# Optimization experiments

Hardware: AMD Instinct MI355X
Metric: run time of the kernel (lower is better)

The kernel has to match this reference:

```python
import jax, jax.numpy as jnp
import numpy as np

SCALE = 32.0 / 16.0  # alpha / r

def setup_inputs() -> dict:
    key = jax.random.key(0)
    k1, k2, k3, k4, k5 = jax.random.split(key, 5)
    B, S, D_in, D_out, R = 4, 4096, 4096, 4096, 16
    x = jax.random.normal(k1, (B, S, D_in), dtype=jnp.float32)
    W = jax.random.normal(k2, (D_out, D_in), dtype=jnp.float32) * 0.02
    b = jax.random.normal(k3, (D_out,), dtype=jnp.float32) * 0.02
    lora_A = jax.random.normal(k4, (D_in, R), dtype=jnp.float32) * 0.01
    lora_B = jax.random.normal(k5, (R, D_out), dtype=jnp.float32) * 0.01
    return {"x": x, "W": W, "b": b, "lora_A": lora_A, "lora_B": lora_B}

def reference(x, W, b, lora_A, lora_B):
    # base: x @ W.T + b  (nn.Linear semantics: weight is [out_f, in_f])
    out = jnp.einsum("bsd,od->bso", x, W) + b
    # LoRA path: (x @ A) @ B, scaled residual add
    lora = jnp.einsum("bsr,ro->bso", jnp.einsum("bsd,dr->bsr", x, lora_A), lora_B)
    return out + SCALE * lora
```

## Files before the change

kernel.cpp:

```cpp
#include <hip/hip_runtime.h>
#include <hip/hip_bf16.h>

typedef __bf16 bf16_t;
typedef __bf16 bf16x8 __attribute__((ext_vector_type(8)));
typedef __bf16 bf16x4 __attribute__((ext_vector_type(4)));
typedef float floatx4 __attribute__((ext_vector_type(4)));

#define M_DIM 16384
#define N_DIM 4096
#define K_DIM 4096
#define R_DIM 16
#define LORA_SCALE 2.0f

__device__ __forceinline__ void async_copy16(void* lds, const void* gptr) {
  __builtin_amdgcn_global_load_lds(
      (__attribute__((address_space(1))) void*)(gptr),
      (__attribute__((address_space(3))) void*)(lds),
      16, 0, 0);
}

__device__ __forceinline__ void block_barrier() {
  asm volatile("" ::: "memory");
  __builtin_amdgcn_s_barrier();
  asm volatile("" ::: "memory");
}

__global__ void cvt_kernel(const float* __restrict__ src,
                           bf16_t* __restrict__ dst, int n8) {
  const int idx = blockIdx.x * blockDim.x + threadIdx.x;
  if (idx >= n8) return;
  const float4 a = ((const float4*)src)[idx * 2 + 0];
  const float4 b = ((const float4*)src)[idx * 2 + 1];
  bf16x8 v;
  v[0] = (bf16_t)a.x; v[1] = (bf16_t)a.y; v[2] = (bf16_t)a.z; v[3] = (bf16_t)a.w;
  v[4] = (bf16_t)b.x; v[5] = (bf16_t)b.y; v[6] = (bf16_t)b.z; v[7] = (bf16_t)b.w;
  ((bf16x8*)dst)[idx] = v;
}

__launch_bounds__(256, 2)
__global__ void lora_xa_bf16(const bf16_t* __restrict__ X,
                             const float* __restrict__ A,
                             bf16_t* __restrict__ T) {
  __shared__ bf16_t Xs[64 * 64];
  __shared__ bf16_t At[16 * 64];
  const int tid  = threadIdx.x;
  const int wave = tid >> 6;
  const int lane = tid & 63;
  const int quad = lane >> 4;
  const int l15  = lane & 15;
  const int gm0  = blockIdx.x * 64;

  floatx4 acc = {0.f, 0.f, 0.f, 0.f};
  for (int k0 = 0; k0 < K_DIM; k0 += 64) {
#pragma unroll
    for (int j = 0; j < 2; ++j) {
      const int i   = wave * 2 + j;
      const int row = i * 8 + (lane >> 3);
      const int col = (lane & 7) * 8;
      async_copy16(&Xs[i * 512], X + (size_t)(gm0 + row) * K_DIM + k0 + col);
    }
    {
      const int c  = tid >> 4;
      const int k4 = (tid & 15) * 4;
#pragma unroll
      for (int j = 0; j < 4; ++j)
        At[c * 64 + k4 + j] = (bf16_t)A[(size_t)(k0 + k4 + j) * R_DIM + c];
    }
    __syncthreads();
#pragma unroll
    for (int h = 0; h < 2; ++h) {
      const int kk = h * 32;
      const bf16x8 a = *(const bf16x8*)&Xs[(wave * 16 + l15) * 64 + kk + quad * 8];
      const bf16x8 b = *(const bf16x8*)&At[l15 * 64 + kk + quad * 8];
      acc = __builtin_amdgcn_mfma_f32_16x16x32_bf16(a, b, acc, 0, 0, 0);
    }
    __syncthreads();
  }
#pragma unroll
  for (int r = 0; r < 4; ++r) {
    const int row = gm0 + wave * 16 + quad * 4 + r;
    T[(size_t)row * R_DIM + l15] = (bf16_t)(LORA_SCALE * acc[r]);
  }
}

__launch_bounds__(256, 2)
__global__ void lora_xa_f32(const float* __restrict__ X,
                            const float* __restrict__ A,
                            bf16_t* __restrict__ T) {
  __shared__ bf16_t Xs[64 * 64];
  __shared__ bf16_t At[16 * 64];
  const int tid  = threadIdx.x;
  const int wave = tid >> 6;
  const int lane = tid & 63;
  const int quad = lane >> 4;
  const int l15  = lane & 15;
  const int gm0  = blockIdx.x * 64;

  floatx4 acc = {0.f, 0.f, 0.f, 0.f};
  for (int k0 = 0; k0 < K_DIM; k0 += 64) {
#pragma unroll
    for (int i = 0; i < 4; ++i) {
      const int idx  = tid + i * 256;
      const int row  = idx >> 4;
      const int colf = idx & 15;
      const float4 v = *(const float4*)&X[(size_t)(gm0 + row) * K_DIM + k0 + colf * 4];
      bf16x4 w;
      w[0] = (bf16_t)v.x; w[1] = (bf16_t)v.y; w[2] = (bf16_t)v.z; w[3] = (bf16_t)v.w;
      *(bf16x4*)&Xs[row * 64 + colf * 4] = w;
    }
    {
      const int c  = tid >> 4;
      const int k4 = (tid & 15) * 4;
#pragma unroll
      for (int j = 0; j < 4; ++j)
        At[c * 64 + k4 + j] = (bf16_t)A[(size_t)(k0 + k4 + j) * R_DIM + c];
    }
    __syncthreads();
#pragma unroll
    for (int h = 0; h < 2; ++h) {
      const int kk = h * 32;
      const bf16x8 a = *(const bf16x8*)&Xs[(wave * 16 + l15) * 64 + kk + quad * 8];
      const bf16x8 b = *(const bf16x8*)&At[l15 * 64 + kk + quad * 8];
      acc = __builtin_amdgcn_mfma_f32_16x16x32_bf16(a, b, acc, 0, 0, 0);
    }
    __syncthreads();
  }
#pragma unroll
  for (int r = 0; r < 4; ++r) {
    const int row = gm0 + wave * 16 + quad * 4 + r;
    T[(size_t)row * R_DIM + l15] = (bf16_t)(LORA_SCALE * acc[r]);
  }
}

#define LD_A(AQ)                                                               \
  _Pragma("unroll") for (int i_ = 0; i_ < 4; ++i_) {                           \
    const int r_ = (rowA + ((AQ) * 4 + i_) * 16) * 64;                         \
    af[i_][0] = *(const bf16x8*)&Ab[r_ + ((quad    ) ^ swz) * 8];              \
    af[i_][1] = *(const bf16x8*)&Ab[r_ + ((quad + 4) ^ swz) * 8];              \
  }

#define LD_B(BQ)                                                               \
  _Pragma("unroll") for (int j_ = 0; j_ < 2; ++j_) {                           \
    const int r_ = (rowB + ((BQ) * 2 + j_) * 16) * 64;                         \
    bfr[j_][0] = *(const bf16x8*)&Bb[r_ + ((quad    ) ^ swz) * 8];             \
    bfr[j_][1] = *(const bf16x8*)&Bb[r_ + ((quad + 4) ^ swz) * 8];             \
  }

#define MFMA16(AQ, BQ)                                                         \
  __builtin_amdgcn_s_setprio(1);                                               \
  _Pragma("unroll") for (int i_ = 0; i_ < 4; ++i_)                             \
  _Pragma("unroll") for (int j_ = 0; j_ < 2; ++j_) {                           \
    acc[(AQ) * 4 + i_][(BQ) * 2 + j_] =                                        \
        __builtin_amdgcn_mfma_f32_16x16x32_bf16(                               \
            af[i_][0], bfr[j_][0], acc[(AQ) * 4 + i_][(BQ) * 2 + j_], 0, 0, 0);\
    acc[(AQ) * 4 + i_][(BQ) * 2 + j_] =                                        \
        __builtin_amdgcn_mfma_f32_16x16x32_bf16(                               \
            af[i_][1], bfr[j_][1], acc[(AQ) * 4 + i_][(BQ) * 2 + j_], 0, 0, 0);\
  }                                                                            \
  __builtin_amdgcn_s_setprio(0);

__launch_bounds__(512, 2)
__global__ void main8_bf16(const bf16_t* __restrict__ X,
                           const bf16_t* __restrict__ W,
                           const float* __restrict__ bias,
                           const float* __restrict__ loraB,
                           const bf16_t* __restrict__ T,
                           float* __restrict__ out) {
  extern __shared__ bf16_t lds[];
  bf16_t* As = lds;
  bf16_t* Bs = lds + 32768;

  const int tid  = threadIdx.x;
  const int wave = tid >> 6;
  const int lane = tid & 63;
  const int quad = lane >> 4;
  const int l15  = lane & 15;
  const int swz  = l15 & 7;
  const int wr   = wave >> 2;
  const int wc   = wave & 3;

  const int b   = blockIdx.x;
  const int swb = (b & 7) * 128 + (b >> 3);
  const int gm  = (swb >> 4) * 256;
  const int gn  = (swb & 15) * 256;

  const int rowA = wr * 128 + l15;
  const int rowB = wc * 64 + l15;

  const int srow  = wave * 8 + (lane >> 3);
  const int sslot = (lane & 7) ^ ((lane >> 3) & 7);
  const bf16_t* gA = X + (size_t)(gm + srow) * K_DIM + sslot * 8;
  const bf16_t* gB = W + (size_t)(gn + srow) * K_DIM + sslot * 8;

  auto stageA = [&](int bsel, int u, int t) {
    async_copy16(As + bsel * 16384 + u * 4096 + wave * 512,
                 gA + (size_t)u * 64 * K_DIM + t * 64);
  };
  auto stageB = [&](int bsel, int u, int t) {
    async_copy16(Bs + bsel * 16384 + u * 4096 + wave * 512,
                 gB + (size_t)u * 64 * K_DIM + t * 64);
  };

  floatx4 acc[8][4];
#pragma unroll
  for (int i = 0; i < 8; ++i)
#pragma unroll
    for (int j = 0; j < 4; ++j) acc[i][j] = (floatx4){0.f, 0.f, 0.f, 0.f};

#pragma unroll
  for (int u = 0; u < 4; ++u) stageA(0, u, 0);
#pragma unroll
  for (int u = 0; u < 4; ++u) stageB(0, u, 0);
  stageA(1, 0, 1); stageA(1, 2, 1);
  asm volatile("s_waitcnt vmcnt(2)" ::: "memory");
  block_barrier();

  const int NITER = K_DIM / 128;
  for (int i = 0; i < NITER; ++i) {
    const int t1 = 2 * i + 1, t2 = 2 * i + 2, t3 = 2 * i + 3;
    const bool last = (i == NITER - 1);
    bf16x8 af[4][2];
    bf16x8 bfr[2][2];

    {
      const bf16_t* Ab = As;
      const bf16_t* Bb = Bs;
      LD_A(0); LD_B(0);
      stageA(1, 1, t1); stageA(1, 3, t1);
      stageB(1, 0, t1); stageB(1, 1, t1); stageB(1, 2, t1); stageB(1, 3, t1);
      block_barrier(); MFMA16(0, 0); block_barrier();
      LD_B(1);
      block_barrier(); MFMA16(0, 1); block_barrier();
      LD_A(1);
      if (!last) { stageA(0, 0, t2); stageA(0, 2, t2); }
      block_barrier(); MFMA16(1, 1); block_barrier();
      LD_B(0);
      block_barrier(); MFMA16(1, 0);
      if (last) asm volatile("s_waitcnt vmcnt(0)" ::: "memory");
      else      asm volatile("s_waitcnt vmcnt(2)" ::: "memory");
      block_barrier();
    }
    {
      const bf16_t* Ab = As + 16384;
      const bf16_t* Bb = Bs + 16384;
      LD_A(0); LD_B(0);
      if (!last) {
        stageA(0, 1, t2); stageA(0, 3, t2);
        stageB(0, 0, t2); stageB(0, 1, t2); stageB(0, 2, t2); stageB(0, 3, t2);
      }
      block_barrier(); MFMA16(0, 0); block_barrier();
      LD_B(1);
      block_barrier(); MFMA16(0, 1); block_barrier();
      LD_A(1);
      if (!last) { stageA(1, 0, t3); stageA(1, 2, t3); }
      block_barrier(); MFMA16(1, 1); block_barrier();
      LD_B(0);
      block_barrier(); MFMA16(1, 0);
      if (last) asm volatile("s_waitcnt vmcnt(0)" ::: "memory");
      else      asm volatile("s_waitcnt vmcnt(2)" ::: "memory");
      block_barrier();
    }
  }

  if (tid < 256) {
    const int row = tid;
    const bf16_t* tp = T + (size_t)(gm + row) * R_DIM;
    *(uint4*)&As[row * 32]      = *(const uint4*)tp;
    *(uint4*)&As[row * 32 + 8]  = *(const uint4*)(tp + 8);
    *(uint4*)&As[row * 32 + 16] = make_uint4(0, 0, 0, 0);
    *(uint4*)&As[row * 32 + 24] = make_uint4(0, 0, 0, 0);
  } else {
    const int n = tid - 256;
#pragma unroll
    for (int r = 0; r < R_DIM; ++r)
      Bs[n * 32 + r] = (bf16_t)loraB[(size_t)r * N_DIM + gn + n];
    *(uint4*)&Bs[n * 32 + 16] = make_uint4(0, 0, 0, 0);
    *(uint4*)&Bs[n * 32 + 24] = make_uint4(0, 0, 0, 0);
  }
  __syncthreads();
  {
    bf16x8 afr[8]; bf16x8 bft[4];
#pragma unroll
    for (int im = 0; im < 8; ++im)
      afr[im] = *(const bf16x8*)&As[(wr * 128 + im * 16 + l15) * 32 + quad * 8];
#pragma unroll
    for (int in = 0; in < 4; ++in)
      bft[in] = *(const bf16x8*)&Bs[(wc * 64 + in * 16 + l15) * 32 + quad * 8];
#pragma unroll
    for (int im = 0; im < 8; ++im)
#pragma unroll
      for (int in = 0; in < 4; ++in)
        acc[im][in] = __builtin_amdgcn_mfma_f32_16x16x32_bf16(
            afr[im], bft[in], acc[im][in], 0, 0, 0);
  }

#pragma unroll
  for (int in = 0; in < 4; ++in) {
    const int col = gn + wc * 64 + in * 16 + l15;
    const float bv = bias[col];
#pragma unroll
    for (int im = 0; im < 8; ++im) {
      const int row0 = gm + wr * 128 + im * 16 + quad * 4;
#pragma unroll
      for (int r = 0; r < 4; ++r)
        out[(size_t)(row0 + r) * N_DIM + col] = acc[im][in][r] + bv;
    }
  }
}

__launch_bounds__(256, 2)
__global__ void main_f32(const float* __restrict__ X,
                         const float* __restrict__ W,
                         const float* __restrict__ bias,
                         const float* __restrict__ loraB,
                         const bf16_t* __restrict__ T,
                         float* __restrict__ out) {
  __shared__ bf16_t As[128 * 32];
  __shared__ bf16_t Bs[128 * 32];
  const int tid  = threadIdx.x;
  const int wave = tid >> 6;
  const int lane = tid & 63;
  const int quad = lane >> 4;
  const int l15  = lane & 15;
  const int gm   = (blockIdx.x >> 5) * 128;
  const int gn   = (blockIdx.x & 31) * 128;
  const int wr   = wave >> 1;
  const int wc   = wave & 1;

  floatx4 acc[4][4];
#pragma unroll
  for (int i = 0; i < 4; ++i)
#pragma unroll
    for (int j = 0; j < 4; ++j) acc[i][j] = (floatx4){0.f, 0.f, 0.f, 0.f};

  for (int k0 = 0; k0 < K_DIM; k0 += 32) {
#pragma unroll
    for (int i = 0; i < 4; ++i) {
      const int idx  = tid + i * 256;
      const int row  = idx >> 3;
      const int colf = idx & 7;
      const float4 va = *(const float4*)&X[(size_t)(gm + row) * K_DIM + k0 + colf * 4];
      const float4 vb = *(const float4*)&W[(size_t)(gn + row) * K_DIM + k0 + colf * 4];
      bf16x4 wa, wb;
      wa[0] = (bf16_t)va.x; wa[1] = (bf16_t)va.y; wa[2] = (bf16_t)va.z; wa[3] = (bf16_t)va.w;
      wb[0] = (bf16_t)vb.x; wb[1] = (bf16_t)vb.y; wb[2] = (bf16_t)vb.z; wb[3] = (bf16_t)vb.w;
      *(bf16x4*)&As[row * 32 + colf * 4] = wa;
      *(bf16x4*)&Bs[row * 32 + colf * 4] = wb;
    }
    __syncthreads();
    bf16x8 a_frag[4], b_frag[4];
#pragma unroll
    for (int im = 0; im < 4; ++im)
      a_frag[im] = *(const bf16x8*)&As[(wr * 64 + im * 16 + l15) * 32 + quad * 8];
#pragma unroll
    for (int in = 0; in < 4; ++in)
      b_frag[in] = *(const bf16x8*)&Bs[(wc * 64 + in * 16 + l15) * 32 + quad * 8];
#pragma unroll
    for (int im = 0; im < 4; ++im)
#pragma unroll
      for (int in = 0; in < 4; ++in)
        acc[im][in] = __builtin_amdgcn_mfma_f32_16x16x32_bf16(
            a_frag[im], b_frag[in], acc[im][in], 0, 0, 0);
    __syncthreads();
  }

  if (tid < 128) {
    const int row = tid;
    const bf16_t* tp = T + (size_t)(gm + row) * R_DIM;
    *(uint4*)&As[row * 32]      = *(const uint4*)tp;
    *(uint4*)&As[row * 32 + 8]  = *(const uint4*)(tp + 8);
    *(uint4*)&As[row * 32 + 16] = make_uint4(0, 0, 0, 0);
    *(uint4*)&As[row * 32 + 24] = make_uint4(0, 0, 0, 0);
  } else {
    const int n = tid - 128;
#pragma unroll
    for (int r = 0; r < R_DIM; ++r)
      Bs[n * 32 + r] = (bf16_t)loraB[(size_t)r * N_DIM + gn + n];
    *(uint4*)&Bs[n * 32 + 16] = make_uint4(0, 0, 0, 0);
    *(uint4*)&Bs[n * 32 + 24] = make_uint4(0, 0, 0, 0);
  }
  __syncthreads();
  {
    bf16x8 a_frag[4], b_frag[4];
#pragma unroll
    for (int im = 0; im < 4; ++im)
      a_frag[im] = *(const bf16x8*)&As[(wr * 64 + im * 16 + l15) * 32 + quad * 8];
#pragma unroll
    for (int in = 0; in < 4; ++in)
      b_frag[in] = *(const bf16x8*)&Bs[(wc * 64 + in * 16 + l15) * 32 + quad * 8];
#pragma unroll
    for (int im = 0; im < 4; ++im)
#pragma unroll
      for (int in = 0; in < 4; ++in)
        acc[im][in] = __builtin_amdgcn_mfma_f32_16x16x32_bf16(
            a_frag[im], b_frag[in], acc[im][in], 0, 0, 0);
  }

#pragma unroll
  for (int in = 0; in < 4; ++in) {
    const int col = gn + wc * 64 + in * 16 + l15;
    const float bv = bias[col];
#pragma unroll
    for (int im = 0; im < 4; ++im) {
      const int row0 = gm + wr * 64 + im * 16 + quad * 4;
#pragma unroll
      for (int r = 0; r < 4; ++r)
        out[(size_t)(row0 + r) * N_DIM + col] = acc[im][in][r] + bv;
    }
  }
}

extern "C" void kernel_launch(void* const* d_in, const int* in_sizes, int n_in,
                              void* d_out, int out_size, void* d_ws, size_t ws_size,
                              hipStream_t stream) {
  const float* X    = (const float*)d_in[0];
  const float* W    = (const float*)d_in[1];
  const float* bias = (const float*)d_in[2];
  const float* lA   = (const float*)d_in[3];
  const float* lB   = (const float*)d_in[4];
  float* out = (float*)d_out;

  bf16_t* T = (bf16_t*)d_ws;
  const size_t offX = 512 * 1024;
  const size_t offW = offX + (size_t)M_DIM * K_DIM * sizeof(bf16_t);
  const size_t need = offW + (size_t)N_DIM * K_DIM * sizeof(bf16_t);

  if (ws_size >= need) {
    bf16_t* Xb = (bf16_t*)((char*)d_ws + offX);
    bf16_t* Wb = (bf16_t*)((char*)d_ws + offW);
    {
      const int n8 = M_DIM * K_DIM / 8;
      cvt_kernel<<<(n8 + 255) / 256, 256, 0, stream>>>(X, Xb, n8);
    }
    {
      const int n8 = N_DIM * K_DIM / 8;
      cvt_kernel<<<(n8 + 255) / 256, 256, 0, stream>>>(W, Wb, n8);
    }
    lora_xa_bf16<<<M_DIM / 64, 256, 0, stream>>>(Xb, lA, T);
    static bool attr_set = false;
    if (!attr_set) {
      (void)hipFuncSetAttribute(reinterpret_cast<const void*>(main8_bf16),
                                hipFuncAttributeMaxDynamicSharedMemorySize,
                                131072);
      attr_set = true;
    }
    main8_bf16<<<(M_DIM / 256) * (N_DIM / 256), 512, 131072, stream>>>(
        Xb, Wb, bias, lB, T, out);
  } else {
    lora_xa_f32<<<M_DIM / 64, 256, 0, stream>>>(X, lA, T);
    main_f32<<<(M_DIM / 128) * (N_DIM / 128), 256, 0, stream>>>(
        X, W, bias, lB, T, out);
  }
}
```

Baseline: 990.2 us.

## Fuse X bf16 conversion into LoRA XA kernel and rebalance main-loop staging

```diff
diff --git a/kernel.cpp b/kernel.cpp
--- a/kernel.cpp
+++ b/kernel.cpp
@@ -38,9 +38,10 @@
 }
 
 __launch_bounds__(256, 2)
-__global__ void lora_xa_bf16(const bf16_t* __restrict__ X,
-                             const float* __restrict__ A,
-                             bf16_t* __restrict__ T) {
+__global__ void lora_xa_cvt(const float* __restrict__ X,
+                            const float* __restrict__ A,
+                            bf16_t* __restrict__ T,
+                            bf16_t* __restrict__ Xb) {
   __shared__ bf16_t Xs[64 * 64];
   __shared__ bf16_t At[16 * 64];
   const int tid  = threadIdx.x;
@@ -53,11 +54,15 @@
   floatx4 acc = {0.f, 0.f, 0.f, 0.f};
   for (int k0 = 0; k0 < K_DIM; k0 += 64) {
 #pragma unroll
-    for (int j = 0; j < 2; ++j) {
-      const int i   = wave * 2 + j;
-      const int row = i * 8 + (lane >> 3);
-      const int col = (lane & 7) * 8;
-      async_copy16(&Xs[i * 512], X + (size_t)(gm0 + row) * K_DIM + k0 + col);
+    for (int i = 0; i < 4; ++i) {
+      const int idx  = tid + i * 256;
+      const int row  = idx >> 4;
+      const int colf = idx & 15;
+      const float4 v = *(const float4*)&X[(size_t)(gm0 + row) * K_DIM + k0 + colf * 4];
+      bf16x4 w;
+      w[0] = (bf16_t)v.x; w[1] = (bf16_t)v.y; w[2] = (bf16_t)v.z; w[3] = (bf16_t)v.w;
+      *(bf16x4*)&Xs[row * 64 + colf * 4] = w;
+      *(bf16x4*)&Xb[(size_t)(gm0 + row) * K_DIM + k0 + colf * 4] = w;
     }
     {
       const int c  = tid >> 4;
@@ -148,15 +153,13 @@
 
 #define MFMA16(AQ, BQ)                                                         \
   __builtin_amdgcn_s_setprio(1);                                               \
+  _Pragma("unroll") for (int h_ = 0; h_ < 2; ++h_)                             \
   _Pragma("unroll") for (int i_ = 0; i_ < 4; ++i_)                             \
-  _Pragma("unroll") for (int j_ = 0; j_ < 2; ++j_) {                           \
+  _Pragma("unroll") for (int j_ = 0; j_ < 2; ++j_)                             \
     acc[(AQ) * 4 + i_][(BQ) * 2 + j_] =                                        \
         __builtin_amdgcn_mfma_f32_16x16x32_bf16(                               \
-            af[i_][0], bfr[j_][0], acc[(AQ) * 4 + i_][(BQ) * 2 + j_], 0, 0, 0);\
-    acc[(AQ) * 4 + i_][(BQ) * 2 + j_] =                                        \
-        __builtin_amdgcn_mfma_f32_16x16x32_bf16(                               \
-            af[i_][1], bfr[j_][1], acc[(AQ) * 4 + i_][(BQ) * 2 + j_], 0, 0, 0);\
-  }                                                                            \
+            af[i_][h_], bfr[j_][h_], acc[(AQ) * 4 + i_][(BQ) * 2 + j_],        \
+            0, 0, 0);                                                          \
   __builtin_amdgcn_s_setprio(0);
 
 __launch_bounds__(512, 2)
@@ -227,14 +230,16 @@
       const bf16_t* Bb = Bs;
       LD_A(0); LD_B(0);
       stageA(1, 1, t1); stageA(1, 3, t1);
-      stageB(1, 0, t1); stageB(1, 1, t1); stageB(1, 2, t1); stageB(1, 3, t1);
+      asm volatile("s_waitcnt lgkmcnt(8)" ::: "memory");
       block_barrier(); MFMA16(0, 0); block_barrier();
       LD_B(1);
+      stageB(1, 0, t1); stageB(1, 1, t1);
       block_barrier(); MFMA16(0, 1); block_barrier();
       LD_A(1);
-      if (!last) { stageA(0, 0, t2); stageA(0, 2, t2); }
+      stageB(1, 2, t1); stageB(1, 3, t1);
       block_barrier(); MFMA16(1, 1); block_barrier();
       LD_B(0);
+      if (!last) { stageA(0, 0, t2); stageA(0, 2, t2); }
       block_barrier(); MFMA16(1, 0);
       if (last) asm volatile("s_waitcnt vmcnt(0)" ::: "memory");
       else      asm volatile("s_waitcnt vmcnt(2)" ::: "memory");
@@ -244,17 +249,17 @@
       const bf16_t* Ab = As + 16384;
       const bf16_t* Bb = Bs + 16384;
       LD_A(0); LD_B(0);
-      if (!last) {
-        stageA(0, 1, t2); stageA(0, 3, t2);
-        stageB(0, 0, t2); stageB(0, 1, t2); stageB(0, 2, t2); stageB(0, 3, t2);
-      }
+      if (!last) { stageA(0, 1, t2); stageA(0, 3, t2); }
+      asm volatile("s_waitcnt lgkmcnt(8)" ::: "memory");
       block_barrier(); MFMA16(0, 0); block_barrier();
       LD_B(1);
+      if (!last) { stageB(0, 0, t2); stageB(0, 1, t2); }
       block_barrier(); MFMA16(0, 1); block_barrier();
       LD_A(1);
-      if (!last) { stageA(1, 0, t3); stageA(1, 2, t3); }
+      if (!last) { stageB(0, 2, t2); stageB(0, 3, t2); }
       block_barrier(); MFMA16(1, 1); block_barrier();
       LD_B(0);
+      if (!last) { stageA(1, 0, t3); stageA(1, 2, t3); }
       block_barrier(); MFMA16(1, 0);
       if (last) asm volatile("s_waitcnt vmcnt(0)" ::: "memory");
       else      asm volatile("s_waitcnt vmcnt(2)" ::: "memory");
@@ -429,14 +434,10 @@
     bf16_t* Xb = (bf16_t*)((char*)d_ws + offX);
     bf16_t* Wb = (bf16_t*)((char*)d_ws + offW);
     {
-      const int n8 = M_DIM * K_DIM / 8;
-      cvt_kernel<<<(n8 + 255) / 256, 256, 0, stream>>>(X, Xb, n8);
-    }
-    {
       const int n8 = N_DIM * K_DIM / 8;
       cvt_kernel<<<(n8 + 255) / 256, 256, 0, stream>>>(W, Wb, n8);
     }
-    lora_xa_bf16<<<M_DIM / 64, 256, 0, stream>>>(Xb, lA, T);
+    lora_xa_cvt<<<M_DIM / 64, 256, 0, stream>>>(X, lA, T, Xb);
     static bool attr_set = false;
     if (!attr_set) {
       (void)hipFuncSetAttribute(reinterpret_cast<const void*>(main8_bf16),
```

New measurement: 967.3 us. 1.02x faster.
